# Performance work log

Hardware: AMD Instinct MI355X
Metric: run time of the kernel (lower is better)

## Reference

```python
import jax, jax.numpy as jnp
import numpy as np

NUM_GRAPHS = 64
NODE_SZ = 200
FEAT = 200
HID = 256          # hidden_size; each signed branch outputs HID//2
HALF = HID // 2
N_NODES = NUM_GRAPHS * NODE_SZ
N_EDGES = 409600
NUM_LAYERS = 3


def _lin_init(key, out_f, in_f):
    kw, kb = jax.random.split(key)
    s = 1.0 / np.sqrt(in_f)
    W = jax.random.uniform(kw, (out_f, in_f), minval=-s, maxval=s, dtype=jnp.float32)
    b = jax.random.uniform(kb, (out_f,), minval=-s, maxval=s, dtype=jnp.float32)
    return W, b


def setup_inputs() -> dict:
    key = jax.random.key(0)
    ks = jax.random.split(key, 16)
    x = jax.random.normal(ks[0], (N_NODES, FEAT), dtype=jnp.float32)
    edge_index = jax.random.randint(ks[1], (2, N_EDGES), 0, N_NODES, dtype=jnp.int64)
    edge_weight = jax.random.normal(ks[2], (N_EDGES,), dtype=jnp.float32)
    batch = jnp.repeat(jnp.arange(NUM_GRAPHS, dtype=jnp.int64), NODE_SZ)

    # signed conv layer params: layer0 in=FEAT, layers 1..: in=HID; each lin maps 2*in -> HALF
    Wp0, bp0 = _lin_init(ks[3], HALF, 2 * FEAT)
    Wn0, bn0 = _lin_init(ks[4], HALF, 2 * FEAT)
    Wp1, bp1 = _lin_init(ks[5], HALF, 2 * HID)
    Wn1, bn1 = _lin_init(ks[6], HALF, 2 * HID)
    Wp2, bp2 = _lin_init(ks[7], HALF, 2 * HID)
    Wn2, bn2 = _lin_init(ks[8], HALF, 2 * HID)
    Wr, br = _lin_init(ks[9], HID, NODE_SZ * HID)   # readout_lin
    Wl, bl = _lin_init(ks[10], 1, HID)              # final lin
    return dict(x=x, edge_index=edge_index, edge_weight=edge_weight, batch=batch,
                Wp0=Wp0, bp0=bp0, Wn0=Wn0, bn0=bn0,
                Wp1=Wp1, bp1=bp1, Wn1=Wn1, bn1=bn1,
                Wp2=Wp2, bp2=bp2, Wn2=Wn2, bn2=bn2,
                Wr=Wr, br=br, Wl=Wl, bl=bl)


def _signed_conv(x, src, dst, w, Wp, bp, Wn, bn):
    # edge-weighted signed mean aggregation, split by weight sign
    xs = x[src]                                   # [E, D] gather
    pw = jnp.where(w > 0, w, 0.0)
    nw = jnp.where(w < 0, -w, 0.0)
    agg_p = jax.ops.segment_sum(pw[:, None] * xs, dst, num_segments=N_NODES)
    agg_n = jax.ops.segment_sum(nw[:, None] * xs, dst, num_segments=N_NODES)
    deg_p = jax.ops.segment_sum((w > 0).astype(x.dtype), dst, num_segments=N_NODES)
    deg_n = jax.ops.segment_sum((w < 0).astype(x.dtype), dst, num_segments=N_NODES)
    agg_p = agg_p / jnp.maximum(deg_p, 1.0)[:, None]
    agg_n = agg_n / jnp.maximum(deg_n, 1.0)[:, None]
    hp = jnp.concatenate([agg_p, x], -1) @ Wp.T + bp
    hn = jnp.concatenate([agg_n, x], -1) @ Wn.T + bn
    return jnp.concatenate([hp, hn], -1)          # [N, HID]


def reference(x, edge_index, edge_weight, batch,
              Wp0, bp0, Wn0, bn0, Wp1, bp1, Wn1, bn1, Wp2, bp2, Wn2, bn2,
              Wr, br, Wl, bl):
    src, dst = edge_index[0], edge_index[1]
    convs = [(Wp0, bp0, Wn0, bn0), (Wp1, bp1, Wn1, bn1), (Wp2, bp2, Wn2, bn2)]
    h = x
    for i, (Wp, bp, Wn, bn) in enumerate(convs):
        h = _signed_conv(h, src, dst, edge_weight, Wp, bp, Wn, bn)
        if i < NUM_LAYERS - 1:
            h = jax.nn.leaky_relu(h, negative_slope=0.01)
    # per-graph readout: batch is contiguous with NODE_SZ nodes per graph,
    # so the boolean-mask+view loop is exactly a reshape.
    g = h.reshape(NUM_GRAPHS, NODE_SZ * HID)
    g = g @ Wr.T + br                             # [G, HID]
    # dropout(p=0.5) is identity in eval mode
    return g @ Wl.T + bl                          # [G, 1]
```

## Files before the change

### kernel.cpp

```cpp
#include <hip/hip_runtime.h>

#define NUM_GRAPHS 64
#define NODE_SZ    200
#define FEAT       200
#define HID        256
#define HALF       128
#define N_NODES    (NUM_GRAPHS * NODE_SZ)
#define KREAD      (NODE_SZ * HID)

typedef unsigned short ushort_t;
typedef unsigned int uint_t;
typedef __attribute__((ext_vector_type(8))) short bf16x8;
typedef __attribute__((ext_vector_type(4))) float f32x4;

#define GAS(p) ((const __attribute__((address_space(1))) void*)(p))
#define LAS(p) ((__attribute__((address_space(3))) void*)(p))

__device__ __forceinline__ float bf2f(ushort_t u) {
    union { unsigned int i; float f; } v; v.i = ((unsigned int)u) << 16; return v.f;
}
__device__ __forceinline__ ushort_t f2bf(float f) {
    union { float f; unsigned int i; } v; v.f = f;
    unsigned int x = v.i;
    unsigned int r = (x + 0x7fffu + ((x >> 16) & 1u)) >> 16;
    return (ushort_t)r;
}

#define OFF_CNT    0
#define OFF_WEFF   51264
#define OFF_ES     256064
#define OFF_YALL   13363264
#define OFF_HA     26470464
#define OFF_HB     33024064
#define OFF_WALL   39577664
#define OFF_XB     40364096

__global__ __launch_bounds__(256) void prep_kernel(
        const float* __restrict__ Wp0, const float* __restrict__ Wn0,
        const float* __restrict__ Wp1, const float* __restrict__ Wn1,
        const float* __restrict__ Wp2, const float* __restrict__ Wn2,
        const float* __restrict__ x, const float* __restrict__ Wr,
        const float* __restrict__ Wl, const float* __restrict__ br,
        const float* __restrict__ bl,
        const int* __restrict__ ei, const float* __restrict__ ew, int E,
        uint_t* __restrict__ cnt, uint2* __restrict__ es,
        ushort_t* __restrict__ wall, ushort_t* __restrict__ xb,
        float* __restrict__ weff, float* __restrict__ outg) {
    int bx = blockIdx.x, tid = threadIdx.x;
    if (bx < 200) {
        int k = bx * 256 + tid;
        float s[16];
#pragma unroll
        for (int j = 0; j < 16; ++j) s[j] = 0.f;
#pragma unroll 1
        for (int c = 0; c < 256; c += 16) {
#pragma unroll
            for (int j = 0; j < 16; ++j)
                s[j] = fmaf(Wl[c + j], Wr[(size_t)(c + j) * KREAD + k], s[j]);
        }
        float t0 = ((s[0] + s[1]) + (s[2] + s[3])) + ((s[4] + s[5]) + (s[6] + s[7]));
        float t1 = ((s[8] + s[9]) + (s[10] + s[11])) + ((s[12] + s[13]) + (s[14] + s[15]));
        weff[k] = t0 + t1;
    } else if (bx < 300) {
        for (int idx = (bx - 200) * 256 + tid; idx < N_NODES * 64; idx += 25600) {
            int n = idx >> 6, c0 = (idx & 63) * 4;
            ushort4 o = {0, 0, 0, 0};
            if (c0 < 200) {
                float4 v = *(const float4*)&x[(size_t)n * 200 + c0];
                o.x = f2bf(v.x); o.y = f2bf(v.y); o.z = f2bf(v.z); o.w = f2bf(v.w);
            }
            *(ushort4*)&xb[(size_t)n * 256 + c0] = o;
        }
    } else if (bx < 364) {
        for (int idx = (bx - 300) * 256 + tid; idx < 3 * 131072; idx += 16384) {
            int layer = idx >> 17, within = idx & 131071;
            int rr = within >> 8, col = within & 255;
            const float* Wp = (layer == 0) ? Wp0 : (layer == 1) ? Wp1 : Wp2;
            const float* Wn = (layer == 0) ? Wn0 : (layer == 1) ? Wn1 : Wn2;
            int Ks = (layer == 0) ? 200 : 256;
            int q = rr >> 7;
            const float* Wsrc = (q & 1) ? Wn : Wp;
            int row = rr & 127;
            int scol = col + ((q >> 1) ? Ks : 0);
            float v = (col < Ks) ? Wsrc[(size_t)row * (2 * Ks) + scol] : 0.0f;
            wall[idx] = f2bf(v);
        }
    } else if (bx < 764) {
        for (int e = (bx - 364) * 256 + tid; e < E; e += 102400) {
            int src = ei[e];
            int dst = ei[E + e];
            float w = ew[e];
            if (w > 0.0f) {
                uint_t old = atomicAdd(&cnt[dst], 1u);
                uint_t rk = old & 0xffffu;
                if (rk < 64u)
                    es[(size_t)dst * 128 + rk] = make_uint2((uint_t)src, __float_as_uint(w));
            } else if (w < 0.0f) {
                uint_t old = atomicAdd(&cnt[dst], 0x10000u);
                uint_t rk = old >> 16;
                if (rk < 64u)
                    es[(size_t)dst * 128 + 64 + rk] = make_uint2((uint_t)src, __float_as_uint(-w));
            }
        }
    } else {
        if (tid < 64) {
            float p = br[tid] * Wl[tid] + br[tid + 64] * Wl[tid + 64]
                    + br[tid + 128] * Wl[tid + 128] + br[tid + 192] * Wl[tid + 192];
#pragma unroll
            for (int d = 32; d > 0; d >>= 1) p += __shfl_xor(p, d);
            outg[tid] = p + bl[0];
        }
    }
}

__global__ __launch_bounds__(512) void gemm_kernel(const ushort_t* __restrict__ A,
                                                   const ushort_t* __restrict__ Bw,
                                                   ushort_t* __restrict__ Y) {
    __shared__ __align__(16) ushort_t smem[20480];
    int t = blockIdx.x;
    int mBase = (t >> 1) * 64;
    int nBase = (t & 1) * 256;
    int tid  = threadIdx.x;
    int lane = tid & 63;
    int wv   = tid >> 6;
    int r    = lane & 15;
    int quad = lane >> 4;
    int wm   = wv >> 2;
    int wn   = wv & 3;

    int rowB = tid >> 2, colc = (tid & 3) * 8;
    const ushort_t* gA  = A  + (size_t)(mBase + (rowB & 63)) * 256 + colc;
    const ushort_t* gB0 = Bw + (size_t)(nBase + rowB) * 256 + colc;
    const ushort_t* gB1 = Bw + (size_t)(nBase + 128 + rowB) * 256 + colc;

    f32x4 acc[2][4];
#pragma unroll
    for (int i = 0; i < 2; ++i)
#pragma unroll
        for (int j = 0; j < 4; ++j) acc[i][j] = (f32x4){0.f, 0.f, 0.f, 0.f};

    auto STAGE = [&](int buf, int kb) {
        if (tid < 256)
            __builtin_amdgcn_global_load_lds(GAS(gA + kb), LAS(smem + (buf << 11) + tid * 8),
                                             16, 0, 0);
        ushort_t* Bd = smem + 4096 + (buf << 13) + tid * 8;
        __builtin_amdgcn_global_load_lds(GAS(gB0 + kb), LAS(Bd), 16, 0, 0);
        __builtin_amdgcn_global_load_lds(GAS(gB1 + kb), LAS(Bd + 4096), 16, 0, 0);
    };

    STAGE(0, 0);
    for (int kt = 0; kt < 8; ++kt) {
        int cb = kt & 1;
        __syncthreads();
        if (kt < 7) STAGE(cb ^ 1, (kt + 1) * 32);
        const ushort_t* Ac = smem + (cb << 11);
        const ushort_t* Bc = smem + 4096 + (cb << 13);
        bf16x8 af[2];
#pragma unroll
        for (int i = 0; i < 2; ++i)
            af[i] = *(const bf16x8*)&Ac[(wm * 32 + i * 16 + r) * 32 + quad * 8];
#pragma unroll
        for (int j = 0; j < 4; ++j) {
            bf16x8 bfr = *(const bf16x8*)&Bc[(wn * 64 + j * 16 + r) * 32 + quad * 8];
            acc[0][j] = __builtin_amdgcn_mfma_f32_16x16x32_bf16(af[0], bfr, acc[0][j], 0, 0, 0);
            acc[1][j] = __builtin_amdgcn_mfma_f32_16x16x32_bf16(af[1], bfr, acc[1][j], 0, 0, 0);
        }
    }
#pragma unroll
    for (int i = 0; i < 2; ++i)
#pragma unroll
        for (int j = 0; j < 4; ++j) {
            int c = nBase + wn * 64 + j * 16 + r;
#pragma unroll
            for (int reg = 0; reg < 4; ++reg) {
                int m = mBase + wm * 32 + i * 16 + quad * 4 + reg;
                Y[(size_t)m * 512 + c] = f2bf(acc[i][j][reg]);
            }
        }
}

template <int B, bool CLAMP>
__device__ __forceinline__ void gather_batch(const uint2* __restrict__ esb,
                                             uint_t e, uint_t hi,
                                             const ushort_t* __restrict__ Yph, int c0,
                                             float* __restrict__ acc) {
    uint_t u[B];
    float  w[B];
#pragma unroll
    for (int j = 0; j < B; ++j) {
        uint_t idx = CLAMP ? min(e + (uint_t)j, hi - 1u) : (e + (uint_t)j);
        uint2 r = esb[idx];
        uint_t s = __builtin_amdgcn_readfirstlane(r.x);
        float  wj = __uint_as_float(r.y);
        w[j] = (CLAMP && (e + (uint_t)j >= hi)) ? 0.0f : wj;
        u[j] = *(const uint_t*)&Yph[(size_t)s * 512 + c0];
    }
#pragma unroll
    for (int j = 0; j < B; ++j) {
        acc[0] = fmaf(w[j], bf2f((ushort_t)(u[j] & 0xffffu)), acc[0]);
        acc[1] = fmaf(w[j], bf2f((ushort_t)(u[j] >> 16)), acc[1]);
    }
}

template <bool LEAKY, bool DOT>
__global__ __launch_bounds__(256) void agg_kernel(
        const ushort_t* __restrict__ Y,
        const uint_t* __restrict__ cnt,
        const uint2* __restrict__ es,
        const float* __restrict__ bp, const float* __restrict__ bn,
        ushort_t* __restrict__ outp,
        const float* __restrict__ weff,
        float* __restrict__ outg) {
    __shared__ float sdot[4];
    int lane = threadIdx.x & 63;
    int wv   = threadIdx.x >> 6;
    int n = blockIdx.x * 4 + wv;
    int c0 = lane * 2;
    uint_t c = __builtin_amdgcn_readfirstlane(cnt[n]);
    uint_t kp = c & 0xffffu, kn = c >> 16;

    float accp[2] = {0.f, 0.f};
    float accn[2] = {0.f, 0.f};

#pragma unroll 1
    for (int phase = 0; phase < 2; ++phase) {
        uint_t hi = phase ? kn : kp;
        const uint2* esb = es + (size_t)n * 128 + (phase ? 64 : 0);
        float* acc = phase ? accn : accp;
        const ushort_t* Yph = Y + (phase ? 128 : 0);
        uint_t e = 0;
#pragma unroll 1
        while (e + 16 <= hi) { gather_batch<16, false>(esb, e, hi, Yph, c0, acc); e += 16; }
        if (e + 8 <= hi)     { gather_batch<8,  false>(esb, e, hi, Yph, c0, acc); e += 8; }
        if (e < hi)          { gather_batch<8,  true >(esb, e, hi, Yph, c0, acc); }
    }

    float dp = fmaxf((float)kp, 1.0f);
    float dn = fmaxf((float)kn, 1.0f);
    float rp = 1.0f / dp, rn = 1.0f / dn;
    uint_t zp = *(const uint_t*)&Y[(size_t)n * 512 + 256 + c0];
    uint_t zn = *(const uint_t*)&Y[(size_t)n * 512 + 384 + c0];
    float vp0 = fmaf(accp[0], rp, bf2f((ushort_t)(zp & 0xffffu)) + bp[c0]);
    float vp1 = fmaf(accp[1], rp, bf2f((ushort_t)(zp >> 16))     + bp[c0 + 1]);
    float vn0 = fmaf(accn[0], rn, bf2f((ushort_t)(zn & 0xffffu)) + bn[c0]);
    float vn1 = fmaf(accn[1], rn, bf2f((ushort_t)(zn >> 16))     + bn[c0 + 1]);
    if (LEAKY) {
        vp0 = (vp0 > 0.0f) ? vp0 : 0.01f * vp0;
        vp1 = (vp1 > 0.0f) ? vp1 : 0.01f * vp1;
        vn0 = (vn0 > 0.0f) ? vn0 : 0.01f * vn0;
        vn1 = (vn1 > 0.0f) ? vn1 : 0.01f * vn1;
    }
    if (DOT) {
        int g = blockIdx.x / 50;
        int kbase = (n % 200) * 256;
        float s = vp0 * weff[kbase + c0] + vp1 * weff[kbase + c0 + 1]
                + vn0 * weff[kbase + 128 + c0] + vn1 * weff[kbase + 128 + c0 + 1];
#pragma unroll
        for (int d = 32; d > 0; d >>= 1) s += __shfl_xor(s, d);
        if (lane == 0) sdot[wv] = s;
        __syncthreads();
        if (threadIdx.x == 0)
            atomicAdd(&outg[g], (sdot[0] + sdot[1]) + (sdot[2] + sdot[3]));
    } else {
        uint_t op = (uint_t)f2bf(vp0) | ((uint_t)f2bf(vp1) << 16);
        uint_t on = (uint_t)f2bf(vn0) | ((uint_t)f2bf(vn1) << 16);
        *(uint_t*)&outp[(size_t)n * 256 + c0]       = op;
        *(uint_t*)&outp[(size_t)n * 256 + 128 + c0] = on;
    }
}

extern "C" void kernel_launch(void* const* d_in, const int* in_sizes, int n_in,
                              void* d_out, int out_size, void* d_ws, size_t ws_size,
                              hipStream_t stream) {
    const float* x  = (const float*)d_in[0];
    const int*   ei = (const int*)d_in[1];
    const float* ew = (const float*)d_in[2];
    const float* Wp0 = (const float*)d_in[4];
    const float* bp0 = (const float*)d_in[5];
    const float* Wn0 = (const float*)d_in[6];
    const float* bn0 = (const float*)d_in[7];
    const float* Wp1 = (const float*)d_in[8];
    const float* bp1 = (const float*)d_in[9];
    const float* Wn1 = (const float*)d_in[10];
    const float* bn1 = (const float*)d_in[11];
    const float* Wp2 = (const float*)d_in[12];
    const float* bp2 = (const float*)d_in[13];
    const float* Wn2 = (const float*)d_in[14];
    const float* bn2 = (const float*)d_in[15];
    const float* Wr  = (const float*)d_in[16];
    const float* br  = (const float*)d_in[17];
    const float* Wl  = (const float*)d_in[18];
    const float* bl  = (const float*)d_in[19];
    const int E = in_sizes[1] / 2;

    char* ws = (char*)d_ws;
    uint_t*   cnt    = (uint_t*)(ws + OFF_CNT);
    float*    weff   = (float*)(ws + OFF_WEFF);
    uint2*    es     = (uint2*)(ws + OFF_ES);
    ushort_t* Yall   = (ushort_t*)(ws + OFF_YALL);
    ushort_t* hA     = (ushort_t*)(ws + OFF_HA);
    ushort_t* hB     = (ushort_t*)(ws + OFF_HB);
    ushort_t* wall   = (ushort_t*)(ws + OFF_WALL);
    ushort_t* xb     = (ushort_t*)(ws + OFF_XB);
    float*    outg   = (float*)d_out;

    hipMemsetAsync(ws + OFF_CNT, 0, N_NODES * sizeof(uint_t), stream);
    hipLaunchKernelGGL(prep_kernel, dim3(765), dim3(256), 0, stream,
                       Wp0, Wn0, Wp1, Wn1, Wp2, Wn2, x, Wr, Wl, br, bl,
                       ei, ew, E, cnt, es, wall, xb, weff, outg);
    hipLaunchKernelGGL(gemm_kernel, dim3(400), dim3(512), 0, stream, xb, wall, Yall);
    hipLaunchKernelGGL((agg_kernel<true, false>), dim3(N_NODES / 4), dim3(256), 0, stream,
                       Yall, cnt, es, bp0, bn0, hA, (const float*)nullptr, (float*)nullptr);
    hipLaunchKernelGGL(gemm_kernel, dim3(400), dim3(512), 0, stream, hA, wall + 131072, Yall);
    hipLaunchKernelGGL((agg_kernel<true, false>), dim3(N_NODES / 4), dim3(256), 0, stream,
                       Yall, cnt, es, bp1, bn1, hB, (const float*)nullptr, (float*)nullptr);
    hipLaunchKernelGGL(gemm_kernel, dim3(400), dim3(512), 0, stream, hB, wall + 262144, Yall);
    hipLaunchKernelGGL((agg_kernel<false, true>), dim3(N_NODES / 4), dim3(256), 0, stream,
                       Yall, cnt, es, bp2, bn2, (ushort_t*)nullptr, weff, outg);
}
```

Before: 281.9 us.

## Move edge bucketing into first GEMM launch and enlarge GEMM M-tile

Edge bucketing (atomic count plus scatter into per-node edge slots) moves out of the prep kernel into a new combined kernel. In that kernel the first 200 blocks run the layer-0 GEMM and the remaining blocks scatter edges, so the scatter can overlap the GEMM. The GEMM tile grows from 64x256 to 128x256 per 512-thread block, giving 200 blocks instead of 400, with each wave holding 2x8 MFMA accumulators. This gives more B reuse per block and fewer, shorter prep-kernel blocks, at the cost of more registers per thread and only 200 blocks to fill the GPU.

```diff
diff --git a/kernel.cpp b/kernel.cpp
--- a/kernel.cpp
+++ b/kernel.cpp
@@ -42,8 +42,6 @@
         const float* __restrict__ x, const float* __restrict__ Wr,
         const float* __restrict__ Wl, const float* __restrict__ br,
         const float* __restrict__ bl,
-        const int* __restrict__ ei, const float* __restrict__ ew, int E,
-        uint_t* __restrict__ cnt, uint2* __restrict__ es,
         ushort_t* __restrict__ wall, ushort_t* __restrict__ xb,
         float* __restrict__ weff, float* __restrict__ outg) {
     int bx = blockIdx.x, tid = threadIdx.x;
@@ -85,23 +83,6 @@
             float v = (col < Ks) ? Wsrc[(size_t)row * (2 * Ks) + scol] : 0.0f;
             wall[idx] = f2bf(v);
         }
-    } else if (bx < 764) {
-        for (int e = (bx - 364) * 256 + tid; e < E; e += 102400) {
-            int src = ei[e];
-            int dst = ei[E + e];
-            float w = ew[e];
-            if (w > 0.0f) {
-                uint_t old = atomicAdd(&cnt[dst], 1u);
-                uint_t rk = old & 0xffffu;
-                if (rk < 64u)
-                    es[(size_t)dst * 128 + rk] = make_uint2((uint_t)src, __float_as_uint(w));
-            } else if (w < 0.0f) {
-                uint_t old = atomicAdd(&cnt[dst], 0x10000u);
-                uint_t rk = old >> 16;
-                if (rk < 64u)
-                    es[(size_t)dst * 128 + 64 + rk] = make_uint2((uint_t)src, __float_as_uint(-w));
-            }
-        }
     } else {
         if (tid < 64) {
             float p = br[tid] * Wl[tid] + br[tid + 64] * Wl[tid + 64]
@@ -113,37 +94,35 @@
     }
 }
 
-__global__ __launch_bounds__(512) void gemm_kernel(const ushort_t* __restrict__ A,
-                                                   const ushort_t* __restrict__ Bw,
-                                                   ushort_t* __restrict__ Y) {
-    __shared__ __align__(16) ushort_t smem[20480];
-    int t = blockIdx.x;
-    int mBase = (t >> 1) * 64;
+__device__ __forceinline__ void gemm_body(int t, const ushort_t* __restrict__ A,
+                                          const ushort_t* __restrict__ Bw,
+                                          ushort_t* __restrict__ Y,
+                                          ushort_t* smem) {
+    int mBase = (t >> 1) * 128;
     int nBase = (t & 1) * 256;
     int tid  = threadIdx.x;
     int lane = tid & 63;
     int wv   = tid >> 6;
     int r    = lane & 15;
     int quad = lane >> 4;
-    int wm   = wv >> 2;
-    int wn   = wv & 3;
-
-    int rowB = tid >> 2, colc = (tid & 3) * 8;
-    const ushort_t* gA  = A  + (size_t)(mBase + (rowB & 63)) * 256 + colc;
-    const ushort_t* gB0 = Bw + (size_t)(nBase + rowB) * 256 + colc;
-    const ushort_t* gB1 = Bw + (size_t)(nBase + 128 + rowB) * 256 + colc;
-
-    f32x4 acc[2][4];
+    int wm   = wv >> 1;
+    int wn   = wv & 1;
+
+    int rowA = tid >> 2, colc = (tid & 3) * 8;
+    const ushort_t* gA  = A  + (size_t)(mBase + rowA) * 256 + colc;
+    const ushort_t* gB0 = Bw + (size_t)(nBase + rowA) * 256 + colc;
+    const ushort_t* gB1 = Bw + (size_t)(nBase + 128 + rowA) * 256 + colc;
+
+    f32x4 acc[2][8];
 #pragma unroll
     for (int i = 0; i < 2; ++i)
 #pragma unroll
-        for (int j = 0; j < 4; ++j) acc[i][j] = (f32x4){0.f, 0.f, 0.f, 0.f};
+        for (int j = 0; j < 8; ++j) acc[i][j] = (f32x4){0.f, 0.f, 0.f, 0.f};
 
     auto STAGE = [&](int buf, int kb) {
-        if (tid < 256)
-            __builtin_amdgcn_global_load_lds(GAS(gA + kb), LAS(smem + (buf << 11) + tid * 8),
-                                             16, 0, 0);
-        ushort_t* Bd = smem + 4096 + (buf << 13) + tid * 8;
+        ushort_t* Ad = smem + (buf << 12) + tid * 8;
+        ushort_t* Bd = smem + 8192 + (buf << 13) + tid * 8;
+        __builtin_amdgcn_global_load_lds(GAS(gA + kb), LAS(Ad), 16, 0, 0);
         __builtin_amdgcn_global_load_lds(GAS(gB0 + kb), LAS(Bd), 16, 0, 0);
         __builtin_amdgcn_global_load_lds(GAS(gB1 + kb), LAS(Bd + 4096), 16, 0, 0);
     };
@@ -153,15 +132,15 @@
         int cb = kt & 1;
         __syncthreads();
         if (kt < 7) STAGE(cb ^ 1, (kt + 1) * 32);
-        const ushort_t* Ac = smem + (cb << 11);
-        const ushort_t* Bc = smem + 4096 + (cb << 13);
+        const ushort_t* Ac = smem + (cb << 12);
+        const ushort_t* Bc = smem + 8192 + (cb << 13);
         bf16x8 af[2];
 #pragma unroll
         for (int i = 0; i < 2; ++i)
             af[i] = *(const bf16x8*)&Ac[(wm * 32 + i * 16 + r) * 32 + quad * 8];
 #pragma unroll
-        for (int j = 0; j < 4; ++j) {
-            bf16x8 bfr = *(const bf16x8*)&Bc[(wn * 64 + j * 16 + r) * 32 + quad * 8];
+        for (int j = 0; j < 8; ++j) {
+            bf16x8 bfr = *(const bf16x8*)&Bc[(wn * 128 + j * 16 + r) * 32 + quad * 8];
             acc[0][j] = __builtin_amdgcn_mfma_f32_16x16x32_bf16(af[0], bfr, acc[0][j], 0, 0, 0);
             acc[1][j] = __builtin_amdgcn_mfma_f32_16x16x32_bf16(af[1], bfr, acc[1][j], 0, 0, 0);
         }
@@ -169,14 +148,51 @@
 #pragma unroll
     for (int i = 0; i < 2; ++i)
 #pragma unroll
-        for (int j = 0; j < 4; ++j) {
-            int c = nBase + wn * 64 + j * 16 + r;
+        for (int j = 0; j < 8; ++j) {
+            int c = nBase + wn * 128 + j * 16 + r;
 #pragma unroll
             for (int reg = 0; reg < 4; ++reg) {
                 int m = mBase + wm * 32 + i * 16 + quad * 4 + reg;
                 Y[(size_t)m * 512 + c] = f2bf(acc[i][j][reg]);
             }
         }
+}
+
+__global__ __launch_bounds__(512) void scatgemm_kernel(
+        const int* __restrict__ ei, const float* __restrict__ ew,
+        uint_t* __restrict__ cnt, uint2* __restrict__ es, int E,
+        const ushort_t* __restrict__ xb, const ushort_t* __restrict__ wall,
+        ushort_t* __restrict__ Yall) {
+    __shared__ __align__(16) ushort_t smem[24576];
+    int bx = blockIdx.x;
+    if (bx < 200) {
+        gemm_body(bx, xb, wall, Yall, smem);
+        return;
+    }
+    int e = (bx - 200) * 512 + threadIdx.x;
+    if (e < E) {
+        int src = ei[e];
+        int dst = ei[E + e];
+        float w = ew[e];
+        if (w > 0.0f) {
+            uint_t old = atomicAdd(&cnt[dst], 1u);
+            uint_t rk = old & 0xffffu;
+            if (rk < 64u)
+                es[(size_t)dst * 128 + rk] = make_uint2((uint_t)src, __float_as_uint(w));
+        } else if (w < 0.0f) {
+            uint_t old = atomicAdd(&cnt[dst], 0x10000u);
+            uint_t rk = old >> 16;
+            if (rk < 64u)
+                es[(size_t)dst * 128 + 64 + rk] = make_uint2((uint_t)src, __float_as_uint(-w));
+        }
+    }
+}
+
+__global__ __launch_bounds__(512) void gemm_kernel(const ushort_t* __restrict__ A,
+                                                   const ushort_t* __restrict__ Bw,
+                                                   ushort_t* __restrict__ Y) {
+    __shared__ __align__(16) ushort_t smem[24576];
+    gemm_body(blockIdx.x, A, Bw, Y, smem);
 }
 
 template <int B, bool CLAMP>
@@ -305,16 +321,17 @@
     float*    outg   = (float*)d_out;
 
     hipMemsetAsync(ws + OFF_CNT, 0, N_NODES * sizeof(uint_t), stream);
-    hipLaunchKernelGGL(prep_kernel, dim3(765), dim3(256), 0, stream,
+    hipLaunchKernelGGL(prep_kernel, dim3(365), dim3(256), 0, stream,
                        Wp0, Wn0, Wp1, Wn1, Wp2, Wn2, x, Wr, Wl, br, bl,
-                       ei, ew, E, cnt, es, wall, xb, weff, outg);
-    hipLaunchKernelGGL(gemm_kernel, dim3(400), dim3(512), 0, stream, xb, wall, Yall);
+                       wall, xb, weff, outg);
+    hipLaunchKernelGGL(scatgemm_kernel, dim3(200 + (E + 511) / 512), dim3(512), 0, stream,
+                       ei, ew, cnt, es, E, xb, wall, Yall);
     hipLaunchKernelGGL((agg_kernel<true, false>), dim3(N_NODES / 4), dim3(256), 0, stream,
                        Yall, cnt, es, bp0, bn0, hA, (const float*)nullptr, (float*)nullptr);
-    hipLaunchKernelGGL(gemm_kernel, dim3(400), dim3(512), 0, stream, hA, wall + 131072, Yall);
+    hipLaunchKernelGGL(gemm_kernel, dim3(200), dim3(512), 0, stream, hA, wall + 131072, Yall);
     hipLaunchKernelGGL((agg_kernel<true, false>), dim3(N_NODES / 4), dim3(256), 0, stream,
                        Yall, cnt, es, bp1, bn1, hB, (const float*)nullptr, (float*)nullptr);
-    hipLaunchKernelGGL(gemm_kernel, dim3(400), dim3(512), 0, stream, hB, wall + 262144, Yall);
+    hipLaunchKernelGGL(gemm_kernel, dim3(200), dim3(512), 0, stream, hB, wall + 262144, Yall);
     hipLaunchKernelGGL((agg_kernel<false, true>), dim3(N_NODES / 4), dim3(256), 0, stream,
                        Yall, cnt, es, bp2, bn2, (ushort_t*)nullptr, weff, outg);
 }
```

Measured after the change: 285.2 us. No clear change (+1.2%).
